# Kernel tuning notes

Measured on AMD Instinct MI355X. Metric: run time of the kernel, lower is better.

## Reference

```python
import jax, jax.numpy as jnp
import numpy as np

C = 512
NUM_GROUPS = 32
EPS = 1e-6


def setup_inputs() -> dict:
    key = jax.random.key(0)
    ks = jax.random.split(key, 6)
    B, H, W = 4, 64, 64
    x = jax.random.normal(ks[0], (B, H, W, C), dtype=jnp.float32)
    # GroupNorm affine params (flax default init: scale=1, bias=0)
    gn_scale = jnp.ones((C,), jnp.float32)
    gn_bias = jnp.zeros((C,), jnp.float32)
    # 1x1 convs == per-pixel dense layers; weight [C_in, C_out], bias [C_out]
    def dense(k):
        return jax.random.normal(k, (C, C), dtype=jnp.float32) * 0.02
    wq, wk, wv, wo = dense(ks[1]), dense(ks[2]), dense(ks[3]), dense(ks[4])
    bq = jnp.zeros((C,), jnp.float32)
    bk = jnp.zeros((C,), jnp.float32)
    bv = jnp.zeros((C,), jnp.float32)
    bo = jnp.zeros((C,), jnp.float32)
    return {"x": x, "gn_scale": gn_scale, "gn_bias": gn_bias,
            "wq": wq, "bq": bq, "wk": wk, "bk": bk,
            "wv": wv, "bv": bv, "wo": wo, "bo": bo}


def _group_norm(x, scale, bias):
    B, H, W, Cc = x.shape
    g = NUM_GROUPS
    xg = x.reshape(B, H, W, g, Cc // g)
    mean = jnp.mean(xg, axis=(1, 2, 4), keepdims=True)
    var = jnp.var(xg, axis=(1, 2, 4), keepdims=True)
    xn = (xg - mean) * jax.lax.rsqrt(var + EPS)
    xn = xn.reshape(B, H, W, Cc)
    return xn * scale + bias


def reference(x, gn_scale, gn_bias, wq, bq, wk, bk, wv, bv, wo, bo):
    B, H, W, Cc = x.shape
    hn = _group_norm(x, gn_scale, gn_bias)
    # 1x1 convs
    q = (hn @ wq + bq).reshape(B, H * W, Cc)
    k = (hn @ wk + bk).reshape(B, H * W, Cc)
    v = (hn @ wv + bv).reshape(B, H * W, Cc)
    scale = jnp.asarray(Cc, x.dtype) ** -0.5
    # scores[b,i,j] = <q_i, k_j> * c^-0.5; softmax over keys j
    attn = jax.nn.softmax(jnp.einsum('bic,bjc->bij', q, k) * scale, axis=-1)
    out = jnp.einsum('bij,bjc->bic', attn, v).reshape(B, H, W, Cc)
    return x + (out @ wo + bo)
```

## Files before the change

kernel.cpp:

```cpp
#include <hip/hip_runtime.h>


typedef __attribute__((ext_vector_type(8))) __bf16 bf16x8;
typedef __attribute__((ext_vector_type(4))) __bf16 bf16x4;
typedef __attribute__((ext_vector_type(4))) float  floatx4;

#define C_DIM 512
#define SPB   4096
#define MTOT  16384

#define HN_OFF  ((size_t)0)
#define Q_OFF   ((size_t)16 << 20)
#define K_OFF   ((size_t)32 << 20)
#define V4_OFF  ((size_t)48 << 20)
#define WT_OFF  ((size_t)64 << 20)
#define O1_OFF  ((size_t)68 << 20)
#define ML_OFF  ((size_t)84 << 20)
#define GS_OFF  (ML_OFF + (size_t)(256 << 10))

__device__ inline floatx4 mfma16(bf16x8 a, bf16x8 b, floatx4 c) {
    return __builtin_amdgcn_mfma_f32_16x16x32_bf16(a, b, c, 0, 0, 0);
}

__device__ inline void gload16(const void* g, void* lds) {
    __builtin_amdgcn_global_load_lds(
        (const __attribute__((address_space(1))) unsigned int*)g,
        (__attribute__((address_space(3))) unsigned int*)lds, 16, 0, 0);
}

__global__ __launch_bounds__(256) void gn_stats(
    const float* __restrict__ x, float* __restrict__ gstats) {
    int bg = blockIdx.x;
    int b = bg >> 5, g = bg & 31;
    int tid = threadIdx.x;
    int cq = tid & 3, s0 = tid >> 2;
    const float* base = x + (size_t)b * SPB * C_DIM + g * 16 + cq * 4
                          + (size_t)blockIdx.y * 1024 * C_DIM;
    float sum = 0.f, sq = 0.f;
#pragma unroll 4
    for (int i = 0; i < 16; ++i) {
        floatx4 v = *(const floatx4*)(base + (size_t)(i * 64 + s0) * C_DIM);
        sum += v[0] + v[1] + v[2] + v[3];
        sq  += v[0]*v[0] + v[1]*v[1] + v[2]*v[2] + v[3]*v[3];
    }
#pragma unroll
    for (int off = 1; off < 64; off <<= 1) {
        sum += __shfl_xor(sum, off);
        sq  += __shfl_xor(sq,  off);
    }
    __shared__ float sm[8];
    int w = tid >> 6, lane = tid & 63;
    if (lane == 0) { sm[w] = sum; sm[4 + w] = sq; }
    __syncthreads();
    if (tid == 0) {
        gstats[(bg * 4 + blockIdx.y) * 2]     = sm[0] + sm[1] + sm[2] + sm[3];
        gstats[(bg * 4 + blockIdx.y) * 2 + 1] = sm[4] + sm[5] + sm[6] + sm[7];
    }
}

__global__ __launch_bounds__(256) void gn_apply(
    const float* __restrict__ x, const float* __restrict__ gstats,
    const float* __restrict__ gsc, const float* __restrict__ gbi,
    __bf16* __restrict__ hn) {
    int bg = blockIdx.x;
    int b = bg >> 5, g = bg & 31;
    int tid = threadIdx.x;
    int cq = tid & 3, s0 = tid >> 2;
    const float* gsB = gstats + bg * 8;
    float S  = gsB[0] + gsB[2] + gsB[4] + gsB[6];
    float Qs = gsB[1] + gsB[3] + gsB[5] + gsB[7];
    float mean = S * (1.f / 65536.f);
    float var  = Qs * (1.f / 65536.f) - mean * mean;
    float rstd = rsqrtf(var + 1e-6f);
    float sc[4], bi[4];
#pragma unroll
    for (int j = 0; j < 4; ++j) {
        float s_ = gsc[g * 16 + cq * 4 + j] * rstd;
        sc[j] = s_;
        bi[j] = gbi[g * 16 + cq * 4 + j] - mean * s_;
    }
    size_t off = (size_t)b * SPB * C_DIM + g * 16 + cq * 4
               + (size_t)blockIdx.y * 1024 * C_DIM;
    const float* base = x + off;
    __bf16* hbase = hn + off;
#pragma unroll 4
    for (int i = 0; i < 16; ++i) {
        floatx4 v = *(const floatx4*)(base + (size_t)(i * 64 + s0) * C_DIM);
        bf16x4 o;
#pragma unroll
        for (int j = 0; j < 4; ++j) o[j] = (__bf16)(v[j] * sc[j] + bi[j]);
        *(bf16x4*)(hbase + (size_t)(i * 64 + s0) * C_DIM) = o;
    }
}

__global__ __launch_bounds__(256) void wt_kernel(
    const float* __restrict__ w0, const float* __restrict__ w1,
    const float* __restrict__ w2, const float* __restrict__ w3,
    __bf16* __restrict__ wt) {
    const float* srcs[4] = {w0, w1, w2, w3};
    const float* src = srcs[blockIdx.z];
    __bf16* dst = wt + (size_t)blockIdx.z * C_DIM * C_DIM;
    __shared__ float tile[32][33];
    int tx = threadIdx.x & 31, ty = threadIdx.x >> 5;
    int gx = blockIdx.x * 32, gy = blockIdx.y * 32;
#pragma unroll
    for (int i = 0; i < 4; ++i)
        tile[ty + i * 8][tx] = src[(size_t)(gy + ty + i * 8) * C_DIM + gx + tx];
    __syncthreads();
#pragma unroll
    for (int i = 0; i < 4; ++i) {
        int n = gx + ty + i * 8;
        int k = gy + tx;
        dst[(size_t)n * C_DIM + k] = (__bf16)tile[tx][ty + i * 8];
    }
}

__global__ __launch_bounds__(256, 2) void proj_qkv(
    const __bf16* __restrict__ hn, const __bf16* __restrict__ wt_all,
    const float* __restrict__ bq, const float* __restrict__ bk,
    const float* __restrict__ bv, __bf16* __restrict__ qout,
    __bf16* __restrict__ kout, __bf16* __restrict__ v4out) {
    int z = blockIdx.z;
    const __bf16* wt = wt_all + (size_t)z * C_DIM * C_DIM;
    const float* bias = (z == 0) ? bq : (z == 1) ? bk : bv;
    __shared__ __bf16 Alds[128 * 32];
    __shared__ __bf16 Blds[128 * 32];
    int tid = threadIdx.x, lane = tid & 63, w = tid >> 6;
    int c = lane & 15, quad = lane >> 4;
    int wm = w & 1, wn = w >> 1;
    int mbase = blockIdx.x * 128, nbase = blockIdx.y * 128;
    floatx4 acc[4][4] = {};
    for (int kb = 0; kb < 16; ++kb) {
        __syncthreads();
#pragma unroll
        for (int p = 0; p < 2; ++p) {
            int chunk0 = w * 128 + p * 64;
            int chunk = chunk0 + lane;
            int row = chunk >> 2, qk = chunk & 3;
            gload16(hn + (size_t)(mbase + row) * C_DIM + kb * 32 + qk * 8, Alds + chunk0 * 8);
            gload16(wt + (size_t)(nbase + row) * C_DIM + kb * 32 + qk * 8, Blds + chunk0 * 8);
        }
        __syncthreads();
        bf16x8 af[4], bfr[4];
#pragma unroll
        for (int mt = 0; mt < 4; ++mt)
            af[mt] = *(const bf16x8*)(Alds + (wm * 64 + mt * 16 + c) * 32 + quad * 8);
#pragma unroll
        for (int nt = 0; nt < 4; ++nt)
            bfr[nt] = *(const bf16x8*)(Blds + (wn * 64 + nt * 16 + c) * 32 + quad * 8);
#pragma unroll
        for (int mt = 0; mt < 4; ++mt)
#pragma unroll
            for (int nt = 0; nt < 4; ++nt)
                acc[mt][nt] = mfma16(af[mt], bfr[nt], acc[mt][nt]);
    }
    if (z == 2) {
        int bb = mbase >> 12;
        int pgbase = (mbase & 4095) >> 3;
        bool qlo = (quad & 1) == 0;
#pragma unroll
        for (int mt = 0; mt < 4; ++mt) {
            int pg = pgbase + wm * 8 + mt * 2 + (quad >> 1);
#pragma unroll
            for (int nt2 = 0; nt2 < 2; ++nt2) {
                int n0 = nbase + wn * 64 + (nt2 * 2) * 16 + c;
                int n1 = n0 + 16;
                float b0 = bias[n0], b1 = bias[n1];
                union { bf16x4 v; unsigned u[2]; } p0, p1;
#pragma unroll
                for (int r = 0; r < 4; ++r) {
                    p0.v[r] = (__bf16)(acc[mt][nt2 * 2][r] + b0);
                    p1.v[r] = (__bf16)(acc[mt][nt2 * 2 + 1][r] + b1);
                }
                unsigned sx = qlo ? p1.u[0] : p0.u[0];
                unsigned sy = qlo ? p1.u[1] : p0.u[1];
                unsigned rx = __shfl_xor(sx, 16);
                unsigned ry = __shfl_xor(sy, 16);
                union { unsigned u[4]; bf16x8 v; } ch;
                if (qlo) { ch.u[0] = p0.u[0]; ch.u[1] = p0.u[1]; ch.u[2] = rx; ch.u[3] = ry; }
                else     { ch.u[0] = rx;      ch.u[1] = ry;      ch.u[2] = p1.u[0]; ch.u[3] = p1.u[1]; }
                int n = qlo ? n0 : n1;
                *(bf16x8*)(v4out + ((size_t)(bb * 512 + pg) * C_DIM + n) * 8) = ch.v;
            }
        }
    } else {
        float scale = (z == 0) ? 0.0441941738241592f : 1.0f;
        __bf16* dst = (z == 0) ? qout : kout;
#pragma unroll
        for (int nt = 0; nt < 4; ++nt) {
            int n = nbase + wn * 64 + nt * 16 + c;
            float bval = bias[n];
#pragma unroll
            for (int mt = 0; mt < 4; ++mt) {
                int m0 = mbase + wm * 64 + mt * 16 + quad * 4;
#pragma unroll
                for (int r = 0; r < 4; ++r) {
                    int m = m0 + r;
                    float val = (acc[mt][nt][r] + bval) * scale;
                    dst[(size_t)m * C_DIM + n] = (__bf16)val;
                }
            }
        }
    }
}

__device__ inline void stage_K(const __bf16* kbase, int key0,
                               __bf16* Klds, int w, int lane) {
#pragma unroll
    for (int p = 0; p < 8; ++p) {
        int chunk0 = w * 512 + p * 64;
        int chunk = chunk0 + lane;
        gload16(kbase + (size_t)(key0 + (chunk & 31)) * C_DIM + (chunk >> 5) * 8,
                Klds + chunk0 * 8);
    }
}

__device__ inline void stage_V(const __bf16* vsrc, __bf16* Vlds, int w, int lane) {
#pragma unroll
    for (int p = 0; p < 8; ++p) {
        int chunk0 = w * 512 + p * 64;
        gload16(vsrc + (size_t)(chunk0 + lane) * 8, Vlds + chunk0 * 8);
    }
}

__global__ __launch_bounds__(256, 2) void flash_kernel(
    const __bf16* __restrict__ q, const __bf16* __restrict__ kmat,
    const __bf16* __restrict__ v4, __bf16* __restrict__ op0,
    __bf16* __restrict__ op1, float* __restrict__ lpart) {
    __shared__ __bf16 Klds[16384];
    __shared__ __bf16 Vlds[16384];
    __shared__ __bf16 Plds[64 * 40];
    int tid = threadIdx.x, lane = tid & 63, w = tid >> 6;
    int c = lane & 15, quad = lane >> 4;
    int bid = blockIdx.x;
    int xcd = bid & 7;
    int b = xcd >> 1, h = xcd & 1, qt = bid >> 3;

    const __bf16* qp = q + ((size_t)(b * SPB + qt * 64 + w * 16 + c)) * C_DIM + quad * 8;
    bf16x8 qf[16];
#pragma unroll
    for (int ks = 0; ks < 16; ++ks) qf[ks] = *(const bf16x8*)(qp + ks * 32);
    floatx4 o[4][8];
#pragma unroll
    for (int mg = 0; mg < 4; ++mg)
#pragma unroll
        for (int t = 0; t < 8; ++t) o[mg][t] = (floatx4){0.f, 0.f, 0.f, 0.f};
    float l_r[4] = {0.f, 0.f, 0.f, 0.f};

    const __bf16* kbase = kmat + (size_t)b * SPB * C_DIM;
    const __bf16* vbase = v4 + (size_t)b * 512 * C_DIM * 8;

    stage_K(kbase, h * 2048, Klds, w, lane);
    __syncthreads();

    for (int kt = 0; kt < 64; ++kt) {
        int key0 = h * 2048 + kt * 32;
        stage_V(vbase + (size_t)(key0 >> 3) * C_DIM * 8, Vlds, w, lane);
        floatx4 s0 = (floatx4){0.f,0.f,0.f,0.f}, s1 = (floatx4){0.f,0.f,0.f,0.f};
#pragma unroll
        for (int ks = 0; ks < 16; ++ks) {
            bf16x8 k0 = *(const bf16x8*)(Klds + (((ks * 4 + quad) * 32) + c) * 8);
            bf16x8 k1 = *(const bf16x8*)(Klds + (((ks * 4 + quad) * 32) + c + 16) * 8);
            s0 = mfma16(qf[ks], k0, s0);
            s1 = mfma16(qf[ks], k1, s1);
        }
#pragma unroll
        for (int r = 0; r < 4; ++r) {
            float p0 = __expf(s0[r]);
            float p1 = __expf(s1[r]);
            l_r[r] += p0 + p1;
            int row = w * 16 + quad * 4 + r;
            Plds[row * 40 + c]      = (__bf16)p0;
            Plds[row * 40 + c + 16] = (__bf16)p1;
        }
        __syncthreads();
        int kn = (kt < 63) ? kt + 1 : 63;
        stage_K(kbase, h * 2048 + kn * 32, Klds, w, lane);
        bf16x8 pf[4];
#pragma unroll
        for (int mg = 0; mg < 4; ++mg)
            pf[mg] = *(const bf16x8*)(Plds + (mg * 16 + c) * 40 + quad * 8);
#pragma unroll
        for (int t = 0; t < 8; ++t) {
            bf16x8 vf = *(const bf16x8*)(Vlds + ((size_t)quad * 512 + w * 128 + t * 16 + c) * 8);
#pragma unroll
            for (int mg = 0; mg < 4; ++mg)
                o[mg][t] = mfma16(pf[mg], vf, o[mg][t]);
        }
        __syncthreads();
    }
#pragma unroll
    for (int r = 0; r < 4; ++r) {
        float l = l_r[r];
        l += __shfl_xor(l, 1);
        l += __shfl_xor(l, 2);
        l += __shfl_xor(l, 4);
        l += __shfl_xor(l, 8);
        l_r[r] = l;
    }
    if (c == 0) {
#pragma unroll
        for (int r = 0; r < 4; ++r) {
            int grow = b * SPB + qt * 64 + w * 16 + quad * 4 + r;
            lpart[h * MTOT + grow] = l_r[r];
        }
    }
    __bf16* ob = h ? op1 : op0;
#pragma unroll
    for (int mg = 0; mg < 4; ++mg)
#pragma unroll
        for (int t = 0; t < 8; ++t)
#pragma unroll
            for (int r = 0; r < 4; ++r) {
                int grow = b * SPB + qt * 64 + mg * 16 + quad * 4 + r;
                ob[(size_t)grow * C_DIM + w * 128 + t * 16 + c] = (__bf16)o[mg][t][r];
            }
}

__global__ __launch_bounds__(256, 2) void proj_out(
    const __bf16* __restrict__ o0, const __bf16* __restrict__ o1,
    const float* __restrict__ lpart, const __bf16* __restrict__ wot,
    const float* __restrict__ bo, const float* __restrict__ x,
    float* __restrict__ out) {
    __shared__ __bf16 Alds[128 * 32];
    __shared__ __bf16 Blds[128 * 32];
    int tid = threadIdx.x, lane = tid & 63, w = tid >> 6;
    int c = lane & 15, quad = lane >> 4;
    int wm = w & 1, wn = w >> 1;
    int mbase = blockIdx.x * 128, nbase = blockIdx.y * 128;
    floatx4 acc[4][4] = {};
    for (int kb = 0; kb < 16; ++kb) {
        __syncthreads();
        bf16x8 a0[2], a1[2];
#pragma unroll
        for (int p = 0; p < 2; ++p) {
            int chunk = w * 128 + p * 64 + lane;
            int row = chunk >> 2, qk = chunk & 3;
            size_t aoff = (size_t)(mbase + row) * C_DIM + kb * 32 + qk * 8;
            a0[p] = *(const bf16x8*)(o0 + aoff);
            a1[p] = *(const bf16x8*)(o1 + aoff);
            gload16(wot + (size_t)(nbase + row) * C_DIM + kb * 32 + qk * 8,
                    Blds + (w * 128 + p * 64) * 8);
        }
#pragma unroll
        for (int p = 0; p < 2; ++p) {
            int chunk = w * 128 + p * 64 + lane;
            bf16x8 s;
#pragma unroll
            for (int j = 0; j < 8; ++j)
                s[j] = (__bf16)((float)a0[p][j] + (float)a1[p][j]);
            *(bf16x8*)(Alds + chunk * 8) = s;
        }
        __syncthreads();
        bf16x8 af[4], bfr[4];
#pragma unroll
        for (int mt = 0; mt < 4; ++mt)
            af[mt] = *(const bf16x8*)(Alds + (wm * 64 + mt * 16 + c) * 32 + quad * 8);
#pragma unroll
        for (int nt = 0; nt < 4; ++nt)
            bfr[nt] = *(const bf16x8*)(Blds + (wn * 64 + nt * 16 + c) * 32 + quad * 8);
#pragma unroll
        for (int mt = 0; mt < 4; ++mt)
#pragma unroll
            for (int nt = 0; nt < 4; ++nt)
                acc[mt][nt] = mfma16(af[mt], bfr[nt], acc[mt][nt]);
    }
    float inv[4][4];
#pragma unroll
    for (int mt = 0; mt < 4; ++mt)
#pragma unroll
        for (int r = 0; r < 4; ++r) {
            int m = mbase + wm * 64 + mt * 16 + quad * 4 + r;
            inv[mt][r] = 1.f / (lpart[m] + lpart[MTOT + m]);
        }
#pragma unroll
    for (int nt = 0; nt < 4; ++nt) {
        int n = nbase + wn * 64 + nt * 16 + c;
        float bval = bo[n];
#pragma unroll
        for (int mt = 0; mt < 4; ++mt) {
            int m0 = mbase + wm * 64 + mt * 16 + quad * 4;
#pragma unroll
            for (int r = 0; r < 4; ++r) {
                size_t idx = (size_t)(m0 + r) * C_DIM + n;
                out[idx] = acc[mt][nt][r] * inv[mt][r] + bval + x[idx];
            }
        }
    }
}

extern "C" void kernel_launch(void* const* d_in, const int* in_sizes, int n_in,
                              void* d_out, int out_size, void* d_ws, size_t ws_size,
                              hipStream_t stream) {
    const float* x   = (const float*)d_in[0];
    const float* gsc = (const float*)d_in[1];
    const float* gbi = (const float*)d_in[2];
    const float* wq  = (const float*)d_in[3];
    const float* bq  = (const float*)d_in[4];
    const float* wk  = (const float*)d_in[5];
    const float* bk  = (const float*)d_in[6];
    const float* wv  = (const float*)d_in[7];
    const float* bv  = (const float*)d_in[8];
    const float* wo  = (const float*)d_in[9];
    const float* bo  = (const float*)d_in[10];
    char* ws = (char*)d_ws;
    __bf16* hn  = (__bf16*)(ws + HN_OFF);
    __bf16* qb  = (__bf16*)(ws + Q_OFF);
    __bf16* kb  = (__bf16*)(ws + K_OFF);
    __bf16* v4  = (__bf16*)(ws + V4_OFF);
    __bf16* wt  = (__bf16*)(ws + WT_OFF);
    __bf16* op0 = (__bf16*)(ws + HN_OFF);
    __bf16* op1 = (__bf16*)(ws + O1_OFF);
    float*  lp  = (float*)(ws + ML_OFF);
    float*  gs  = (float*)(ws + GS_OFF);
    float* out = (float*)d_out;

    wt_kernel<<<dim3(16, 16, 4), 256, 0, stream>>>(wq, wk, wv, wo, wt);
    gn_stats<<<dim3(128, 4), 256, 0, stream>>>(x, gs);
    gn_apply<<<dim3(128, 4), 256, 0, stream>>>(x, gs, gsc, gbi, hn);
    proj_qkv<<<dim3(128, 4, 3), 256, 0, stream>>>(hn, wt, bq, bk, bv, qb, kb, v4);
    flash_kernel<<<512, 256, 0, stream>>>(qb, kb, v4, op0, op1, lp);
    proj_out<<<dim3(128, 4), 256, 0, stream>>>(op0, op1, lp,
        wt + (size_t)3 * C_DIM * C_DIM, bo, x, out);
}
```

Measured before the change: 411.8 us.

## Restructure GroupNorm kernels to read full contiguous rows per block

Before, each GroupNorm block read only a 16-channel (64-byte) slice of every spatial row, which gives poorly coalesced strided loads. Now each block covers 32 full spatial rows across all 512 channels and writes per-chunk partial sums for all 32 groups. gn_apply reduces those 128 partials per group in shared memory before normalising. This makes global reads and writes contiguous, at the cost of a larger partial-stats buffer and an extra reduction step in gn_apply.

```diff
diff --git a/kernel.cpp b/kernel.cpp
--- a/kernel.cpp
+++ b/kernel.cpp
@@ -30,31 +30,30 @@
 
 __global__ __launch_bounds__(256) void gn_stats(
     const float* __restrict__ x, float* __restrict__ gstats) {
-    int bg = blockIdx.x;
-    int b = bg >> 5, g = bg & 31;
-    int tid = threadIdx.x;
-    int cq = tid & 3, s0 = tid >> 2;
-    const float* base = x + (size_t)b * SPB * C_DIM + g * 16 + cq * 4
-                          + (size_t)blockIdx.y * 1024 * C_DIM;
-    float sum = 0.f, sq = 0.f;
+    int bc = blockIdx.x;
+    int b = bc >> 7, chunk = bc & 127;
+    int t = threadIdx.x;
+    int rh = t >> 7, cl = t & 127;
+    const float* base = x + (size_t)(b * SPB + chunk * 32 + rh) * C_DIM + cl * 4;
+    float s = 0.f, q = 0.f;
 #pragma unroll 4
     for (int i = 0; i < 16; ++i) {
-        floatx4 v = *(const floatx4*)(base + (size_t)(i * 64 + s0) * C_DIM);
-        sum += v[0] + v[1] + v[2] + v[3];
-        sq  += v[0]*v[0] + v[1]*v[1] + v[2]*v[2] + v[3]*v[3];
-    }
-#pragma unroll
-    for (int off = 1; off < 64; off <<= 1) {
-        sum += __shfl_xor(sum, off);
-        sq  += __shfl_xor(sq,  off);
-    }
-    __shared__ float sm[8];
-    int w = tid >> 6, lane = tid & 63;
-    if (lane == 0) { sm[w] = sum; sm[4 + w] = sq; }
+        floatx4 v = *(const floatx4*)(base + (size_t)(i * 2) * C_DIM);
+        s += v[0] + v[1] + v[2] + v[3];
+        q += v[0]*v[0] + v[1]*v[1] + v[2]*v[2] + v[3]*v[3];
+    }
+    __shared__ float smS[256], smQ[256];
+    smS[t] = s; smQ[t] = q;
     __syncthreads();
-    if (tid == 0) {
-        gstats[(bg * 4 + blockIdx.y) * 2]     = sm[0] + sm[1] + sm[2] + sm[3];
-        gstats[(bg * 4 + blockIdx.y) * 2 + 1] = sm[4] + sm[5] + sm[6] + sm[7];
+    if (t < 32) {
+        float S = 0.f, Q = 0.f;
+#pragma unroll
+        for (int j = 0; j < 4; ++j) {
+            S += smS[t * 4 + j] + smS[128 + t * 4 + j];
+            Q += smQ[t * 4 + j] + smQ[128 + t * 4 + j];
+        }
+        gstats[((size_t)bc * 32 + t) * 2]     = S;
+        gstats[((size_t)bc * 32 + t) * 2 + 1] = Q;
     }
 }
 
@@ -62,34 +61,53 @@
     const float* __restrict__ x, const float* __restrict__ gstats,
     const float* __restrict__ gsc, const float* __restrict__ gbi,
     __bf16* __restrict__ hn) {
-    int bg = blockIdx.x;
-    int b = bg >> 5, g = bg & 31;
-    int tid = threadIdx.x;
-    int cq = tid & 3, s0 = tid >> 2;
-    const float* gsB = gstats + bg * 8;
-    float S  = gsB[0] + gsB[2] + gsB[4] + gsB[6];
-    float Qs = gsB[1] + gsB[3] + gsB[5] + gsB[7];
-    float mean = S * (1.f / 65536.f);
-    float var  = Qs * (1.f / 65536.f) - mean * mean;
-    float rstd = rsqrtf(var + 1e-6f);
+    int bc = blockIdx.x;
+    int b = bc >> 7, chunk = bc & 127;
+    int t = threadIdx.x;
+    int rh = t >> 7, cl = t & 127;
+    int g = cl >> 2;
+    __shared__ float smS[8][32], smQ[8][32], smMean[32], smRstd[32];
+    {
+        int gg = t & 31, s8 = t >> 5;
+        float S = 0.f, Q = 0.f;
+        const float* gsB = gstats + (size_t)b * 128 * 64;
+#pragma unroll 4
+        for (int k = 0; k < 16; ++k) {
+            int cch = s8 + k * 8;
+            S += gsB[(cch * 32 + gg) * 2];
+            Q += gsB[(cch * 32 + gg) * 2 + 1];
+        }
+        smS[s8][gg] = S; smQ[s8][gg] = Q;
+    }
+    __syncthreads();
+    if (t < 32) {
+        float S = 0.f, Q = 0.f;
+#pragma unroll
+        for (int s8 = 0; s8 < 8; ++s8) { S += smS[s8][t]; Q += smQ[s8][t]; }
+        float mean = S * (1.f / 65536.f);
+        float var  = Q * (1.f / 65536.f) - mean * mean;
+        smMean[t] = mean;
+        smRstd[t] = rsqrtf(var + 1e-6f);
+    }
+    __syncthreads();
+    float mean = smMean[g], rstd = smRstd[g];
     float sc[4], bi[4];
 #pragma unroll
     for (int j = 0; j < 4; ++j) {
-        float s_ = gsc[g * 16 + cq * 4 + j] * rstd;
+        float s_ = gsc[cl * 4 + j] * rstd;
         sc[j] = s_;
-        bi[j] = gbi[g * 16 + cq * 4 + j] - mean * s_;
-    }
-    size_t off = (size_t)b * SPB * C_DIM + g * 16 + cq * 4
-               + (size_t)blockIdx.y * 1024 * C_DIM;
+        bi[j] = gbi[cl * 4 + j] - mean * s_;
+    }
+    size_t off = (size_t)(b * SPB + chunk * 32 + rh) * C_DIM + cl * 4;
     const float* base = x + off;
     __bf16* hbase = hn + off;
 #pragma unroll 4
     for (int i = 0; i < 16; ++i) {
-        floatx4 v = *(const floatx4*)(base + (size_t)(i * 64 + s0) * C_DIM);
+        floatx4 v = *(const floatx4*)(base + (size_t)(i * 2) * C_DIM);
         bf16x4 o;
 #pragma unroll
         for (int j = 0; j < 4; ++j) o[j] = (__bf16)(v[j] * sc[j] + bi[j]);
-        *(bf16x4*)(hbase + (size_t)(i * 64 + s0) * C_DIM) = o;
+        *(bf16x4*)(hbase + (size_t)(i * 2) * C_DIM) = o;
     }
 }
 
@@ -416,8 +434,8 @@
     float* out = (float*)d_out;
 
     wt_kernel<<<dim3(16, 16, 4), 256, 0, stream>>>(wq, wk, wv, wo, wt);
-    gn_stats<<<dim3(128, 4), 256, 0, stream>>>(x, gs);
-    gn_apply<<<dim3(128, 4), 256, 0, stream>>>(x, gs, gsc, gbi, hn);
+    gn_stats<<<512, 256, 0, stream>>>(x, gs);
+    gn_apply<<<512, 256, 0, stream>>>(x, gs, gsc, gbi, hn);
     proj_qkv<<<dim3(128, 4, 3), 256, 0, stream>>>(hn, wt, bq, bk, bv, qb, kb, v4);
     flash_kernel<<<512, 256, 0, stream>>>(qb, kb, v4, op0, op1, lp);
     proj_out<<<dim3(128, 4), 256, 0, stream>>>(op0, op1, lp,
```

Result: no change. 405.8 us (-1.5%).
